# Performance work log

Hardware: AMD Instinct MI355X
Metric: run time of the kernel (lower is better)

## Reference

```python
import jax, jax.numpy as jnp
import numpy as np

STRIDES = [8, 16, 32, 64, 128]
CLASS_NUM = 80
SCORE_THR = 0.05
IOU_THR = 0.6
MAX_DET = 1000


def setup_inputs() -> dict:
    key = jax.random.key(0)
    ks = jax.random.split(key, 16)
    B, H, W = 8, 1024, 1024
    inp = {}
    for i, s in enumerate(STRIDES):
        h, w = H // s, W // s
        inp[f"cls_p{i+3}"] = jax.random.normal(ks[i], (B, CLASS_NUM, h, w), jnp.float32)
        inp[f"cnt_p{i+3}"] = jax.random.normal(ks[5 + i], (B, 1, h, w), jnp.float32)
        # ltrb offsets are positive distances; scale by stride for realistic boxes
        inp[f"reg_p{i+3}"] = jax.random.uniform(ks[10 + i], (B, 4, h, w), jnp.float32) * (4.0 * s)
    inp["batch_imgs"] = jax.random.normal(ks[15], (B, 3, H, W), jnp.float32)
    return inp


def _reshape_cat(levels):
    # [B,c,h,w] -> [B,sum(h*w),c], matching permute(0,2,3,1).reshape
    B, c = levels[0].shape[0], levels[0].shape[1]
    return jnp.concatenate([jnp.transpose(p, (0, 2, 3, 1)).reshape(B, -1, c) for p in levels], axis=1)


def _coords(levels):
    cs = []
    for p, s in zip(levels, STRIDES):
        h, w = p.shape[2], p.shape[3]
        sx = jnp.arange(w, dtype=jnp.float32) * s
        sy = jnp.arange(h, dtype=jnp.float32) * s
        yy, xx = jnp.meshgrid(sy, sx, indexing='ij')
        cs.append(jnp.stack([xx.ravel(), yy.ravel()], axis=-1) + s // 2)
    return jnp.concatenate(cs, axis=0)  # [sum(h*w),2]


def _nms_keep(boxes, scores, classes, valid, iou_thr):
    # boxes [M,4] already sorted by descending score; greedy class-offset NMS
    maxc = jnp.max(boxes)
    off = classes.astype(boxes.dtype) * (maxc + 1.0)
    b = boxes + off[:, None]
    x1, y1, x2, y2 = b[:, 0], b[:, 1], b[:, 2], b[:, 3]
    areas = (x2 - x1 + 1.0) * (y2 - y1 + 1.0)
    xx1 = jnp.maximum(x1[:, None], x1[None, :])
    yy1 = jnp.maximum(y1[:, None], y1[None, :])
    xx2 = jnp.minimum(x2[:, None], x2[None, :])
    yy2 = jnp.minimum(y2[:, None], y2[None, :])
    inter = jnp.maximum(xx2 - xx1, 0.0) * jnp.maximum(yy2 - yy1, 0.0)
    iou = inter / (areas[:, None] + areas[None, :] - inter)  # [M,M]
    M = boxes.shape[0]
    idx = jnp.arange(M)

    def body(i, keep):
        sup = jnp.any(keep & (iou[:, i] > iou_thr) & (idx < i))
        return keep.at[i].set(valid[i] & jnp.logical_not(sup))

    return jax.lax.fori_loop(0, M, body, jnp.zeros((M,), dtype=bool))


def reference(cls_p3, cls_p4, cls_p5, cls_p6, cls_p7,
              cnt_p3, cnt_p4, cnt_p5, cnt_p6, cnt_p7,
              reg_p3, reg_p4, reg_p5, reg_p6, reg_p7,
              batch_imgs):
    cls_levels = [cls_p3, cls_p4, cls_p5, cls_p6, cls_p7]
    cnt_levels = [cnt_p3, cnt_p4, cnt_p5, cnt_p6, cnt_p7]
    reg_levels = [reg_p3, reg_p4, reg_p5, reg_p6, reg_p7]

    cls_logits = _reshape_cat(cls_levels)     # [B,N,C]
    cnt_logits = _reshape_cat(cnt_levels)     # [B,N,1]
    reg_preds = _reshape_cat(reg_levels)      # [B,N,4]
    coords = _coords(cls_levels)              # [N,2]

    cls_preds = jax.nn.sigmoid(cls_logits)
    cnt_preds = jax.nn.sigmoid(cnt_logits)
    cls_scores = jnp.max(cls_preds, axis=-1)                    # [B,N]
    cls_classes = jnp.argmax(cls_preds, axis=-1) + 1            # [B,N]
    cls_scores = jnp.sqrt(cls_scores * cnt_preds[..., 0])       # add_centerness

    # ltrb offsets -> xyxy boxes
    boxes = jnp.concatenate([coords[None] - reg_preds[..., :2],
                             coords[None] + reg_preds[..., 2:]], axis=-1)  # [B,N,4]

    max_num = min(MAX_DET, cls_scores.shape[-1])
    topk_scores, topk_ind = jax.lax.top_k(cls_scores, max_num)             # sorted desc
    topk_classes = jnp.take_along_axis(cls_classes, topk_ind, axis=1)
    topk_boxes = jnp.take_along_axis(boxes, topk_ind[..., None], axis=1)

    valid = topk_scores >= SCORE_THR
    keep = jax.vmap(lambda b, s, c, v: _nms_keep(b, s, c, v, IOU_THR))(
        topk_boxes, topk_scores, topk_classes, valid)                      # [B,max_num]

    # ClipBoxes
    h, w = batch_imgs.shape[2], batch_imgs.shape[3]
    cb = jnp.maximum(topk_boxes, 0.0)
    xs = jnp.minimum(cb[..., 0::2], float(w - 1))
    ys = jnp.minimum(cb[..., 1::2], float(h - 1))
    cb = jnp.stack([xs[..., 0], ys[..., 0], xs[..., 1], ys[..., 1]], axis=-1)

    scores_out = jnp.where(keep, topk_scores, 0.0)
    classes_out = jnp.where(keep, topk_classes, 0)
    boxes_out = jnp.where(keep[..., None], cb, 0.0)
    return scores_out, classes_out, boxes_out
```

## Files before the change

kernel.cpp:

```cpp
#include <hip/hip_runtime.h>
#include <stdint.h>

#define NLOC   21824
#define NQUAD  5456
#define BATCH  8
#define MAXDET 1000
#define NCLS   80

struct LevelPtrs {
    const float* cls[5];
    const float* cnt[5];
    const float* reg[5];
};

__global__ __launch_bounds__(256) void k_stage1(LevelPtrs lp, float* scores,
                                                int* cls_out, float4* boxes) {
    __shared__ float4 bl4[8][32];
    __shared__ int4   bc4[8][32];
    int tid = threadIdx.x;
    int p   = tid >> 5;
    int qq  = tid & 31;
    int blk = blockIdx.x;
    int b   = blockIdx.y;

    int lvl, qoff, logw, strd;
    if (blk < 128)      { lvl = 0; qoff = 0;    logw = 7; strd = 8;   }
    else if (blk < 160) { lvl = 1; qoff = 4096; logw = 6; strd = 16;  }
    else if (blk < 168) { lvl = 2; qoff = 5120; logw = 5; strd = 32;  }
    else if (blk < 170) { lvl = 3; qoff = 5376; logw = 4; strd = 64;  }
    else                { lvl = 4; qoff = 5440; logw = 3; strd = 128; }

    int quad  = blk * 32 + qq;
    bool valid = quad < NQUAD;
    int ql   = quad - qoff;
    int loc  = ql * 4;
    int hw   = 1 << (2 * logw);
    int hw4  = hw >> 2;

    float bl[4] = {-3.0e38f, -3.0e38f, -3.0e38f, -3.0e38f};
    int   bc[4] = {0, 0, 0, 0};
    if (valid) {
        const float4* cp = (const float4*)(lp.cls[lvl] + (size_t)(b * NCLS) * hw + loc);
        int c0 = p * 10;
#pragma unroll
        for (int g = 0; g < 2; ++g) {
            float4 lv[5];
#pragma unroll
            for (int k = 0; k < 5; ++k)
                lv[k] = cp[(size_t)(c0 + g * 5 + k) * hw4];
#pragma unroll
            for (int k = 0; k < 5; ++k) {
                int c = c0 + g * 5 + k;
                const float* lf = (const float*)&lv[k];
#pragma unroll
                for (int u = 0; u < 4; ++u)
                    if (lf[u] > bl[u]) { bl[u] = lf[u]; bc[u] = c; }
            }
        }
    }
    bl4[p][qq] = make_float4(bl[0], bl[1], bl[2], bl[3]);
    bc4[p][qq] = make_int4(bc[0], bc[1], bc[2], bc[3]);
    __syncthreads();

    if (tid < 32 && valid) {
        int q = tid;
        float4 B = bl4[0][q]; int4 C = bc4[0][q];
        float bestl[4] = {B.x, B.y, B.z, B.w};
        int   bestc[4] = {C.x, C.y, C.z, C.w};
#pragma unroll
        for (int pp = 1; pp < 8; ++pp) {
            float4 Bp = bl4[pp][q]; int4 Cp = bc4[pp][q];
            const float* bf = (const float*)&Bp;
            const int*   cf = (const int*)&Cp;
#pragma unroll
            for (int u = 0; u < 4; ++u)
                if (bf[u] > bestl[u]) { bestl[u] = bf[u]; bestc[u] = cf[u]; }
        }

        float4 lcv = *(const float4*)(lp.cnt[lvl] + (size_t)b * hw + loc);
        const float* lc = (const float*)&lcv;

        const float4* rp = (const float4*)(lp.reg[lvl] + (size_t)(b * 4) * hw + loc);
        float4 r0v = rp[0], r1v = rp[hw4], r2v = rp[2 * hw4], r3v = rp[3 * hw4];
        const float* r0 = (const float*)&r0v;
        const float* r1 = (const float*)&r1v;
        const float* r2 = (const float*)&r2v;
        const float* r3 = (const float*)&r3v;

        int x = loc & ((1 << logw) - 1);
        int y = loc >> logw;
        float cy = (float)(y * strd + (strd >> 1));

        float sc4[4]; int cl4[4]; float4 bx4[4];
#pragma unroll
        for (int u = 0; u < 4; ++u) {
            float e = expf(-bestl[u]);
            float sig_cls = 1.0f / (1.0f + e);
            float sig_cnt = 1.0f / (1.0f + expf(-lc[u]));
            sc4[u] = sqrtf(__fmul_rn(sig_cls, sig_cnt));
            cl4[u] = bestc[u] + 1;
            float cx = (float)((x + u) * strd + (strd >> 1));
            bx4[u] = make_float4(__fsub_rn(cx, r0[u]), __fsub_rn(cy, r1[u]),
                                 __fadd_rn(cx, r2[u]), __fadd_rn(cy, r3[u]));
        }

        int o = b * NLOC + quad * 4;
        *(float4*)(scores + o) = make_float4(sc4[0], sc4[1], sc4[2], sc4[3]);
        *(int4*)(cls_out + o)  = make_int4(cl4[0], cl4[1], cl4[2], cl4[3]);
#pragma unroll
        for (int u = 0; u < 4; ++u) boxes[o + u] = bx4[u];
    }
}

__global__ __launch_bounds__(1024) void k_select(const uint32_t* scores_u,
                                                 const float4* boxes,
                                                 const int* cls_ws,
                                                 float* topk_score, float4* gbox,
                                                 int* gcls, float4* obox,
                                                 float* areas, uint64_t* nzmask) {
    __shared__ uint32_t hist[256];
    __shared__ uint32_t cum[256];
    __shared__ uint64_t keys[2048];
    __shared__ uint32_t prefix_sh, cnt_sh;
    __shared__ int R_sh;
    __shared__ float redmax[16];
    __shared__ float maxc_sh;

    int b = blockIdx.x, tid = threadIdx.x;
    if (tid < 16) nzmask[b * 16 + tid] = 0;
    const uint4* sc4 = (const uint4*)(scores_u + (size_t)b * NLOC);

    uint32_t prefix = 0;
    int R = MAXDET;
    for (int d = 3; d >= 0; --d) {
        if (tid < 256) hist[tid] = 0;
        __syncthreads();
        int shl = 8 * d;
        int last = -1; uint32_t run = 0;
        for (int n4 = tid; n4 < NQUAD; n4 += 1024) {
            uint4 v = sc4[n4];
            uint32_t vals[4] = {v.x, v.y, v.z, v.w};
#pragma unroll
            for (int u = 0; u < 4; ++u) {
                uint32_t sb = vals[u];
                bool m = (d == 3) || ((sb >> (shl + 8)) == prefix);
                int dig = m ? (int)((sb >> shl) & 255u) : -1;
                if (dig != last) {
                    if (last >= 0 && run) atomicAdd(&hist[last], run);
                    last = dig; run = 0;
                }
                if (dig >= 0) run++;
            }
        }
        if (last >= 0 && run) atomicAdd(&hist[last], run);
        __syncthreads();

        if (tid < 256) cum[tid] = hist[tid];
        __syncthreads();
        for (int st = 1; st < 256; st <<= 1) {
            uint32_t v = 0;
            if (tid < 256) v = cum[tid] + ((tid + st < 256) ? cum[tid + st] : 0);
            __syncthreads();
            if (tid < 256) cum[tid] = v;
            __syncthreads();
        }
        if (tid < 256) {
            uint32_t cge  = cum[tid];
            uint32_t cge1 = (tid < 255) ? cum[tid + 1] : 0;
            if (cge >= (uint32_t)R && cge1 < (uint32_t)R) {
                prefix_sh = (prefix << 8) | (uint32_t)tid;
                R_sh = R - (int)cge1;
            }
        }
        __syncthreads();
        prefix = prefix_sh;
        R = R_sh;
        __syncthreads();
    }
    uint32_t Sstar = prefix;

    if (tid == 0) cnt_sh = 0;
    __syncthreads();
    for (int n4 = tid; n4 < NQUAD; n4 += 1024) {
        uint4 v = sc4[n4];
        uint32_t vals[4] = {v.x, v.y, v.z, v.w};
#pragma unroll
        for (int u = 0; u < 4; ++u) {
            uint32_t sb = vals[u];
            if (sb >= Sstar) {
                uint32_t n = (uint32_t)(n4 * 4 + u);
                uint32_t slot = atomicAdd(&cnt_sh, 1u);
                if (slot < 2048)
                    keys[slot] = ((uint64_t)sb << 32) | (uint32_t)(~n);
            }
        }
    }
    __syncthreads();
    uint32_t cnt = cnt_sh > 2048u ? 2048u : cnt_sh;

    uint64_t myk0 = 0, myk1 = 0;
    bool has0 = tid < (int)cnt, has1 = (tid + 1024) < (int)cnt;
    if (has0) myk0 = keys[tid];
    if (has1) myk1 = keys[tid + 1024];
    int rk0 = 0, rk1 = 0;
    for (uint32_t j = 0; j < cnt; ++j) {
        uint64_t kj = keys[j];
        rk0 += (kj > myk0);
        rk1 += (kj > myk1);
    }

    float lmax = -3.0e38f;
    float4 v0, v1; int cl0 = 0, cl1 = 0; bool k0 = false, k1 = false;
    if (has0 && rk0 < MAXDET) {
        uint32_t n = ~(uint32_t)myk0;
        v0 = boxes[(size_t)b * NLOC + n];
        cl0 = cls_ws[(size_t)b * NLOC + n];
        topk_score[b * MAXDET + rk0] = __uint_as_float((uint32_t)(myk0 >> 32));
        gbox[b * MAXDET + rk0] = v0;
        gcls[b * MAXDET + rk0] = cl0;
        lmax = fmaxf(fmaxf(v0.x, v0.y), fmaxf(v0.z, v0.w));
        k0 = true;
    }
    if (has1 && rk1 < MAXDET) {
        uint32_t n = ~(uint32_t)myk1;
        v1 = boxes[(size_t)b * NLOC + n];
        cl1 = cls_ws[(size_t)b * NLOC + n];
        topk_score[b * MAXDET + rk1] = __uint_as_float((uint32_t)(myk1 >> 32));
        gbox[b * MAXDET + rk1] = v1;
        gcls[b * MAXDET + rk1] = cl1;
        lmax = fmaxf(lmax, fmaxf(fmaxf(v1.x, v1.y), fmaxf(v1.z, v1.w)));
        k1 = true;
    }

#pragma unroll
    for (int off = 32; off > 0; off >>= 1)
        lmax = fmaxf(lmax, __shfl_down(lmax, off, 64));
    if ((tid & 63) == 0) redmax[tid >> 6] = lmax;
    __syncthreads();
    if (tid == 0) {
        float m = redmax[0];
        for (int w = 1; w < 16; ++w) m = fmaxf(m, redmax[w]);
        maxc_sh = __fadd_rn(m, 1.0f);
    }
    __syncthreads();
    float maxc1 = maxc_sh;

    if (k0) {
        float off0 = __fmul_rn((float)cl0, maxc1);
        float4 o = make_float4(__fadd_rn(v0.x, off0), __fadd_rn(v0.y, off0),
                               __fadd_rn(v0.z, off0), __fadd_rn(v0.w, off0));
        obox[b * MAXDET + rk0] = o;
        areas[b * MAXDET + rk0] =
            __fmul_rn(__fadd_rn(__fsub_rn(o.z, o.x), 1.0f),
                      __fadd_rn(__fsub_rn(o.w, o.y), 1.0f));
    }
    if (k1) {
        float off1 = __fmul_rn((float)cl1, maxc1);
        float4 o = make_float4(__fadd_rn(v1.x, off1), __fadd_rn(v1.y, off1),
                               __fadd_rn(v1.z, off1), __fadd_rn(v1.w, off1));
        obox[b * MAXDET + rk1] = o;
        areas[b * MAXDET + rk1] =
            __fmul_rn(__fadd_rn(__fsub_rn(o.z, o.x), 1.0f),
                      __fadd_rn(__fsub_rn(o.w, o.y), 1.0f));
    }
}

__global__ __launch_bounds__(256) void k_iou(const float4* obox, const float* areas,
                                             uint64_t* rows, uint64_t* nzmask) {
    __shared__ float4 ob[MAXDET];
    __shared__ float  ca[MAXDET];
    __shared__ uint64_t nzloc[16];
    int b = blockIdx.x, word = blockIdx.y, tid = threadIdx.x;
    if (tid < 16) nzloc[tid] = 0;
    for (int r = tid; r < MAXDET; r += 256) {
        ob[r] = obox[b * MAXDET + r];
        ca[r] = areas[b * MAXDET + r];
    }
    __syncthreads();

    int j0 = word * 64;
    int jlim = MAXDET - j0;
    if (jlim > 64) jlim = 64;

#pragma unroll
    for (int qr = 0; qr < 4; ++qr) {
        int i = tid + qr * 256;
        if (i >= MAXDET) continue;
        uint64_t rw = 0;
        int jmax = j0 + jlim;
        if (i < jmax - 1) {
            float4 bi = ob[i];
            float ai = ca[i];
            for (int jj = 0; jj < jlim; ++jj) {
                int j = j0 + jj;
                float4 bj = ob[j0 + jj];
                float xx1 = fmaxf(bi.x, bj.x), yy1 = fmaxf(bi.y, bj.y);
                float xx2 = fminf(bi.z, bj.z), yy2 = fminf(bi.w, bj.w);
                float w_ = fmaxf(__fsub_rn(xx2, xx1), 0.0f);
                float h_ = fmaxf(__fsub_rn(yy2, yy1), 0.0f);
                float inter = __fmul_rn(w_, h_);
                float denom = __fsub_rn(__fadd_rn(ai, ca[j0 + jj]), inter);
                bool sup = (j > i) && (inter > __fmul_rn(0.6f, denom));
                rw |= sup ? (1ull << jj) : 0ull;
            }
        }
        rows[((size_t)(b * MAXDET) + i) * 16 + word] = rw;
        if (rw) atomicOr(&nzloc[i >> 6], 1ull << (i & 63));
    }
    __syncthreads();
    if (tid < 16 && nzloc[tid])
        atomicOr(&nzmask[b * 16 + tid], nzloc[tid]);
}

__global__ __launch_bounds__(256) void k_nms_out(const uint64_t* rows,
                                                 const uint64_t* nzmask,
                                                 const float* topk_score,
                                                 const int* gcls, const float4* gbox,
                                                 float* out) {
    __shared__ uint64_t validmask[16];
    __shared__ uint64_t keepmask[16];
    __shared__ int zlist[MAXDET];
    __shared__ int m_sh;
    int b = blockIdx.x, tid = threadIdx.x;

    if (tid < 16) validmask[tid] = 0;
    if (tid == 0) m_sh = 0;
    __syncthreads();
    for (int r = tid; r < MAXDET; r += 256)
        if (topk_score[b * MAXDET + r] >= 0.05f)
            atomicOr(&validmask[r >> 6], 1ull << (r & 63));
    if (tid == 0) {
        int m = 0;
        for (int w = 0; w < 16; ++w) {
            uint64_t nz = nzmask[b * 16 + w];
            while (nz) {
                int bit = __ffsll((unsigned long long)nz) - 1;
                nz &= nz - 1;
                zlist[m++] = w * 64 + bit;
            }
        }
        m_sh = m;
    }
    __syncthreads();

    int m = m_sh;
    uint64_t S = 0, V = 0;
    if (tid < 16) V = validmask[tid];
    if (tid < 64) {
        const uint64_t* rg = rows + (size_t)b * MAXDET * 16;
        uint64_t row_nxt = 0;
        if (m > 0 && tid < 16) row_nxt = rg[(size_t)zlist[0] * 16 + tid];
        for (int k = 0; k < m; ++k) {
            uint64_t row_cur = row_nxt;
            if (k + 1 < m && tid < 16)
                row_nxt = rg[(size_t)zlist[k + 1] * 16 + tid];
            int z = zlist[k];
            int w = z >> 6, bp = z & 63;
            uint32_t aliveV = ((uint32_t)(V >> bp) & ~(uint32_t)(S >> bp)) & 1u;
            uint32_t alive = (uint32_t)__builtin_amdgcn_readlane((int)aliveV, w);
            if (alive) S |= row_cur;
        }
    }
    if (tid < 16) keepmask[tid] = V & ~S;
    __syncthreads();

    for (int r = tid; r < MAXDET; r += 256) {
        bool keep = ((keepmask[r >> 6] >> (r & 63)) & 1ull) != 0;
        float sc = topk_score[b * MAXDET + r];
        int cl = gcls[b * MAXDET + r];
        float4 v = gbox[b * MAXDET + r];
        float c0 = fminf(fmaxf(v.x, 0.0f), 1023.0f);
        float c1 = fminf(fmaxf(v.y, 0.0f), 1023.0f);
        float c2 = fminf(fmaxf(v.z, 0.0f), 1023.0f);
        float c3 = fminf(fmaxf(v.w, 0.0f), 1023.0f);
        out[b * MAXDET + r] = keep ? sc : 0.0f;
        out[BATCH * MAXDET + b * MAXDET + r] = keep ? (float)cl : 0.0f;
        float4* op = (float4*)(out + 2 * BATCH * MAXDET) + (b * MAXDET + r);
        *op = keep ? make_float4(c0, c1, c2, c3) : make_float4(0.f, 0.f, 0.f, 0.f);
    }
}

extern "C" void kernel_launch(void* const* d_in, const int* in_sizes, int n_in,
                              void* d_out, int out_size, void* d_ws, size_t ws_size,
                              hipStream_t stream) {
    (void)in_sizes; (void)n_in; (void)out_size; (void)ws_size;

    LevelPtrs lp;
    for (int i = 0; i < 5; ++i) {
        lp.cls[i] = (const float*)d_in[3 * i + 0];
        lp.cnt[i] = (const float*)d_in[3 * i + 1];
        lp.reg[i] = (const float*)d_in[3 * i + 2];
    }

    char* ws = (char*)d_ws;
    float*    scores   = (float*)   (ws + 0);
    int*      cls_ws   = (int*)     (ws + 698368);
    float4*   boxes    = (float4*)  (ws + 1396736);
    float*    topk_sc  = (float*)   (ws + 4222208);
    int*      gcls     = (int*)     (ws + 4254208);
    float4*   gbox     = (float4*)  (ws + 4286208);
    float4*   obox     = (float4*)  (ws + 4414208);
    float*    areas    = (float*)   (ws + 4542208);
    uint64_t* rows     = (uint64_t*)(ws + 4574208);
    uint64_t* nzmask   = (uint64_t*)(ws + 5598208);

    dim3 g1(171, BATCH);
    k_stage1<<<g1, 256, 0, stream>>>(lp, scores, cls_ws, boxes);

    k_select<<<BATCH, 1024, 0, stream>>>((const uint32_t*)scores, boxes, cls_ws,
                                         topk_sc, gbox, gcls, obox, areas, nzmask);

    dim3 g4(BATCH, 16);
    k_iou<<<g4, 256, 0, stream>>>(obox, areas, rows, nzmask);

    k_nms_out<<<BATCH, 256, 0, stream>>>(rows, nzmask, topk_sc, gcls, gbox,
                                         (float*)d_out);
}
```

Baseline: 271.9 us.

## Cache scores in registers, wave-scan histogram, unroll rank loop, stage NMS rows in LDS

k_select now loads each block's scores into registers once and reuses them across all four radix passes and the candidate gather, instead of re-reading global memory five times. The 256-bin suffix scan becomes a single-wavefront shuffle scan, removing the barrier-heavy loop and one sync per pass. The rank counting is unrolled by eight with zero padding, and the second key is skipped when there are few candidates. k_nms_out first copies up to 448 nonzero suppression rows into shared memory in parallel so the serial greedy loop reads LDS rather than dependent global loads, at the cost of about 57 KB of LDS per block.

Result: faster. 253.7 us (median of 2 runs) (-6.7%).

```diff
diff --git a/kernel.cpp b/kernel.cpp
--- a/kernel.cpp
+++ b/kernel.cpp
@@ -118,9 +118,8 @@
                                                  float* topk_score, float4* gbox,
                                                  int* gcls, float4* obox,
                                                  float* areas, uint64_t* nzmask) {
-    __shared__ uint32_t hist[256];
-    __shared__ uint32_t cum[256];
-    __shared__ uint64_t keys[2048];
+    __shared__ __align__(16) uint32_t hist[256];
+    __shared__ uint64_t keys[2048 + 8];
     __shared__ uint32_t prefix_sh, cnt_sh;
     __shared__ int R_sh;
     __shared__ float redmax[16];
@@ -128,7 +127,16 @@
 
     int b = blockIdx.x, tid = threadIdx.x;
     if (tid < 16) nzmask[b * 16 + tid] = 0;
+    if (tid == 0) cnt_sh = 0;
     const uint4* sc4 = (const uint4*)(scores_u + (size_t)b * NLOC);
+
+    uint4 sv[6];
+#pragma unroll
+    for (int it = 0; it < 6; ++it) {
+        int n4 = tid + it * 1024;
+        sv[it] = make_uint4(0u, 0u, 0u, 0u);
+        if (n4 < NQUAD) sv[it] = sc4[n4];
+    }
 
     uint32_t prefix = 0;
     int R = MAXDET;
@@ -137,99 +145,118 @@
         __syncthreads();
         int shl = 8 * d;
         int last = -1; uint32_t run = 0;
-        for (int n4 = tid; n4 < NQUAD; n4 += 1024) {
-            uint4 v = sc4[n4];
-            uint32_t vals[4] = {v.x, v.y, v.z, v.w};
-#pragma unroll
-            for (int u = 0; u < 4; ++u) {
-                uint32_t sb = vals[u];
-                bool m = (d == 3) || ((sb >> (shl + 8)) == prefix);
-                int dig = m ? (int)((sb >> shl) & 255u) : -1;
-                if (dig != last) {
-                    if (last >= 0 && run) atomicAdd(&hist[last], run);
-                    last = dig; run = 0;
+#pragma unroll
+        for (int it = 0; it < 6; ++it) {
+            if (tid + it * 1024 < NQUAD) {
+                uint32_t vals[4] = {sv[it].x, sv[it].y, sv[it].z, sv[it].w};
+#pragma unroll
+                for (int u = 0; u < 4; ++u) {
+                    uint32_t sb = vals[u];
+                    bool m = (d == 3) || ((sb >> (shl + 8)) == prefix);
+                    int dig = m ? (int)((sb >> shl) & 255u) : -1;
+                    if (dig != last) {
+                        if (last >= 0 && run) atomicAdd(&hist[last], run);
+                        last = dig; run = 0;
+                    }
+                    if (dig >= 0) run++;
                 }
-                if (dig >= 0) run++;
             }
         }
         if (last >= 0 && run) atomicAdd(&hist[last], run);
         __syncthreads();
 
-        if (tid < 256) cum[tid] = hist[tid];
-        __syncthreads();
-        for (int st = 1; st < 256; st <<= 1) {
-            uint32_t v = 0;
-            if (tid < 256) v = cum[tid] + ((tid + st < 256) ? cum[tid + st] : 0);
-            __syncthreads();
-            if (tid < 256) cum[tid] = v;
-            __syncthreads();
-        }
-        if (tid < 256) {
-            uint32_t cge  = cum[tid];
-            uint32_t cge1 = (tid < 255) ? cum[tid + 1] : 0;
-            if (cge >= (uint32_t)R && cge1 < (uint32_t)R) {
-                prefix_sh = (prefix << 8) | (uint32_t)tid;
-                R_sh = R - (int)cge1;
+        if (tid < 64) {
+            uint4 h4 = *(const uint4*)&hist[tid * 4];
+            uint32_t s3 = h4.w;
+            uint32_t s2 = h4.z + s3;
+            uint32_t s1 = h4.y + s2;
+            uint32_t s0 = h4.x + s1;
+            uint32_t acc = s0;
+#pragma unroll
+            for (int off = 1; off < 64; off <<= 1) {
+                uint32_t t = __shfl_down(acc, off, 64);
+                if (tid + off < 64) acc += t;
+            }
+            uint32_t above = acc - s0;
+            uint32_t cge [4] = {above + s0, above + s1, above + s2, above + s3};
+            uint32_t cge1[4] = {above + s1, above + s2, above + s3, above};
+#pragma unroll
+            for (int u = 0; u < 4; ++u) {
+                if (cge[u] >= (uint32_t)R && cge1[u] < (uint32_t)R) {
+                    prefix_sh = (prefix << 8) | (uint32_t)(tid * 4 + u);
+                    R_sh = R - (int)cge1[u];
+                }
             }
         }
         __syncthreads();
         prefix = prefix_sh;
         R = R_sh;
-        __syncthreads();
     }
     uint32_t Sstar = prefix;
 
-    if (tid == 0) cnt_sh = 0;
-    __syncthreads();
-    for (int n4 = tid; n4 < NQUAD; n4 += 1024) {
-        uint4 v = sc4[n4];
-        uint32_t vals[4] = {v.x, v.y, v.z, v.w};
-#pragma unroll
-        for (int u = 0; u < 4; ++u) {
-            uint32_t sb = vals[u];
-            if (sb >= Sstar) {
-                uint32_t n = (uint32_t)(n4 * 4 + u);
-                uint32_t slot = atomicAdd(&cnt_sh, 1u);
-                if (slot < 2048)
-                    keys[slot] = ((uint64_t)sb << 32) | (uint32_t)(~n);
+#pragma unroll
+    for (int it = 0; it < 6; ++it) {
+        if (tid + it * 1024 < NQUAD) {
+            uint32_t vals[4] = {sv[it].x, sv[it].y, sv[it].z, sv[it].w};
+#pragma unroll
+            for (int u = 0; u < 4; ++u) {
+                uint32_t sb = vals[u];
+                if (sb >= Sstar) {
+                    uint32_t n = (uint32_t)((tid + it * 1024) * 4 + u);
+                    uint32_t slot = atomicAdd(&cnt_sh, 1u);
+                    if (slot < 2048)
+                        keys[slot] = ((uint64_t)sb << 32) | (uint32_t)(~n);
+                }
             }
         }
     }
     __syncthreads();
     uint32_t cnt = cnt_sh > 2048u ? 2048u : cnt_sh;
-
-    uint64_t myk0 = 0, myk1 = 0;
-    bool has0 = tid < (int)cnt, has1 = (tid + 1024) < (int)cnt;
-    if (has0) myk0 = keys[tid];
-    if (has1) myk1 = keys[tid + 1024];
-    int rk0 = 0, rk1 = 0;
-    for (uint32_t j = 0; j < cnt; ++j) {
-        uint64_t kj = keys[j];
-        rk0 += (kj > myk0);
-        rk1 += (kj > myk1);
-    }
+    if (tid < 8) keys[cnt + tid] = 0;
+    __syncthreads();
 
     float lmax = -3.0e38f;
     float4 v0, v1; int cl0 = 0, cl1 = 0; bool k0 = false, k1 = false;
-    if (has0 && rk0 < MAXDET) {
-        uint32_t n = ~(uint32_t)myk0;
-        v0 = boxes[(size_t)b * NLOC + n];
-        cl0 = cls_ws[(size_t)b * NLOC + n];
-        topk_score[b * MAXDET + rk0] = __uint_as_float((uint32_t)(myk0 >> 32));
-        gbox[b * MAXDET + rk0] = v0;
-        gcls[b * MAXDET + rk0] = cl0;
-        lmax = fmaxf(fmaxf(v0.x, v0.y), fmaxf(v0.z, v0.w));
-        k0 = true;
-    }
-    if (has1 && rk1 < MAXDET) {
-        uint32_t n = ~(uint32_t)myk1;
-        v1 = boxes[(size_t)b * NLOC + n];
-        cl1 = cls_ws[(size_t)b * NLOC + n];
-        topk_score[b * MAXDET + rk1] = __uint_as_float((uint32_t)(myk1 >> 32));
-        gbox[b * MAXDET + rk1] = v1;
-        gcls[b * MAXDET + rk1] = cl1;
-        lmax = fmaxf(lmax, fmaxf(fmaxf(v1.x, v1.y), fmaxf(v1.z, v1.w)));
-        k1 = true;
+    int rk0 = 0, rk1 = 0;
+    uint64_t myk0 = 0, myk1 = 0;
+
+    if (tid < (int)cnt) {
+        myk0 = keys[tid];
+        for (int j = 0; j < (int)cnt; j += 8) {
+            uint64_t a0 = keys[j + 0], a1 = keys[j + 1], a2 = keys[j + 2], a3 = keys[j + 3];
+            uint64_t a4 = keys[j + 4], a5 = keys[j + 5], a6 = keys[j + 6], a7 = keys[j + 7];
+            rk0 += (int)(a0 > myk0) + (int)(a1 > myk0) + (int)(a2 > myk0) + (int)(a3 > myk0)
+                 + (int)(a4 > myk0) + (int)(a5 > myk0) + (int)(a6 > myk0) + (int)(a7 > myk0);
+        }
+        if (rk0 < MAXDET) {
+            uint32_t n = ~(uint32_t)myk0;
+            v0 = boxes[(size_t)b * NLOC + n];
+            cl0 = cls_ws[(size_t)b * NLOC + n];
+            topk_score[b * MAXDET + rk0] = __uint_as_float((uint32_t)(myk0 >> 32));
+            gbox[b * MAXDET + rk0] = v0;
+            gcls[b * MAXDET + rk0] = cl0;
+            lmax = fmaxf(fmaxf(v0.x, v0.y), fmaxf(v0.z, v0.w));
+            k0 = true;
+        }
+    }
+    if ((int)cnt > 1024 && tid + 1024 < (int)cnt) {
+        myk1 = keys[tid + 1024];
+        for (int j = 0; j < (int)cnt; j += 8) {
+            uint64_t a0 = keys[j + 0], a1 = keys[j + 1], a2 = keys[j + 2], a3 = keys[j + 3];
+            uint64_t a4 = keys[j + 4], a5 = keys[j + 5], a6 = keys[j + 6], a7 = keys[j + 7];
+            rk1 += (int)(a0 > myk1) + (int)(a1 > myk1) + (int)(a2 > myk1) + (int)(a3 > myk1)
+                 + (int)(a4 > myk1) + (int)(a5 > myk1) + (int)(a6 > myk1) + (int)(a7 > myk1);
+        }
+        if (rk1 < MAXDET) {
+            uint32_t n = ~(uint32_t)myk1;
+            v1 = boxes[(size_t)b * NLOC + n];
+            cl1 = cls_ws[(size_t)b * NLOC + n];
+            topk_score[b * MAXDET + rk1] = __uint_as_float((uint32_t)(myk1 >> 32));
+            gbox[b * MAXDET + rk1] = v1;
+            gcls[b * MAXDET + rk1] = cl1;
+            lmax = fmaxf(lmax, fmaxf(fmaxf(v1.x, v1.y), fmaxf(v1.z, v1.w)));
+            k1 = true;
+        }
     }
 
 #pragma unroll
@@ -312,6 +339,8 @@
         atomicOr(&nzmask[b * 16 + tid], nzloc[tid]);
 }
 
+#define NZSTG 448
+
 __global__ __launch_bounds__(256) void k_nms_out(const uint64_t* rows,
                                                  const uint64_t* nzmask,
                                                  const float* topk_score,
@@ -321,6 +350,7 @@
     __shared__ uint64_t keepmask[16];
     __shared__ int zlist[MAXDET];
     __shared__ int m_sh;
+    __shared__ uint64_t srow[NZSTG * 16];
     int b = blockIdx.x, tid = threadIdx.x;
 
     if (tid < 16) validmask[tid] = 0;
@@ -344,16 +374,25 @@
     __syncthreads();
 
     int m = m_sh;
+    int ms = m < NZSTG ? m : NZSTG;
+    const uint64_t* rg = rows + (size_t)b * MAXDET * 16;
+
+    for (int idx = tid; idx < ms * 16; idx += 256)
+        srow[idx] = rg[(size_t)zlist[idx >> 4] * 16 + (idx & 15)];
+    __syncthreads();
+
     uint64_t S = 0, V = 0;
     if (tid < 16) V = validmask[tid];
     if (tid < 64) {
-        const uint64_t* rg = rows + (size_t)b * MAXDET * 16;
         uint64_t row_nxt = 0;
-        if (m > 0 && tid < 16) row_nxt = rg[(size_t)zlist[0] * 16 + tid];
+        if (m > 0 && tid < 16)
+            row_nxt = (0 < ms) ? srow[tid] : rg[(size_t)zlist[0] * 16 + tid];
         for (int k = 0; k < m; ++k) {
             uint64_t row_cur = row_nxt;
-            if (k + 1 < m && tid < 16)
-                row_nxt = rg[(size_t)zlist[k + 1] * 16 + tid];
+            int kn = k + 1;
+            if (kn < m && tid < 16)
+                row_nxt = (kn < ms) ? srow[kn * 16 + tid]
+                                    : rg[(size_t)zlist[kn] * 16 + tid];
             int z = zlist[k];
             int w = z >> 6, bp = z & 63;
             uint32_t aliveV = ((uint32_t)(V >> bp) & ~(uint32_t)(S >> bp)) & 1u;
```
